# Kernel optimization log

Measured on AMD Instinct MI355X. Metric: run time of the kernel, lower is better.

## Reference

```python
import jax, jax.numpy as jnp
import numpy as np

PAD_IDX = 1
B, L, E, H = 2, 256, 512, 8
D = E // H
SCALE = D ** -0.5


def setup_inputs() -> dict:
    key = jax.random.key(0)
    ks = jax.random.split(key, 10)
    std = 0.02
    return {
        "queries": jax.random.normal(ks[0], (B, L, E), jnp.float32),
        "keys": jax.random.normal(ks[1], (B, L, E), jnp.float32),
        "values": jax.random.normal(ks[2], (B, L, E), jnp.float32),
        "relation": jax.random.normal(ks[3], (B, L, L, E), jnp.float32),
        "adj_mask": jax.random.randint(ks[4], (B, L, L), 0, 2, jnp.int32),
        "Wq": jax.random.normal(ks[5], (E, E), jnp.float32) * std,
        "bq": jnp.zeros((E,), jnp.float32),
        "Wk": jax.random.normal(ks[6], (E, E), jnp.float32) * std,
        "bk": jnp.zeros((E,), jnp.float32),
        "Wv": jax.random.normal(ks[7], (E, E), jnp.float32) * std,
        "bv": jnp.zeros((E,), jnp.float32),
        "Wr": jax.random.normal(ks[8], (2 * E, E), jnp.float32) * std,
        "Wo": jax.random.normal(ks[9], (E, E), jnp.float32) * std,
        "bo": jnp.zeros((E,), jnp.float32),
    }


def reference(queries, keys, values, relation, adj_mask,
              Wq, bq, Wk, bk, Wv, bv, Wr, Wo, bo):
    b, t, _ = queries.shape
    s = keys.shape[1]
    # input projections (torch Linear: y = x @ W.T + b)
    q = ((queries @ Wq.T + bq) * SCALE).reshape(b, t, H, D)
    k = (keys @ Wk.T + bk).reshape(b, s, H, D)
    v = (values @ Wv.T + bv).reshape(b, s, H, D)
    # relation projection -> relation queries/keys, [b, t, s, H, D] then transpose(1,2)
    rel = relation @ Wr.T                              # [b, t, s, 2E]
    rq, rk = jnp.split(rel, 2, axis=-1)
    rq = rq.reshape(b, t, s, H, D).transpose(0, 2, 1, 3, 4)  # [b, s, t, H, D]
    rk = rk.reshape(b, t, s, H, D).transpose(0, 2, 1, 3, 4)
    # broadcasted relation bias (requires t == s, as in the original)
    qe = q[:, :, None] + rq                            # [b, t, s, H, D]
    ke = k[:, None] + rk                               # [b, t, s, H, D]
    attn = jnp.einsum('bijhn,bijhn->bijh', qe, ke)     # [b, t, s, H]
    pad = (adj_mask == PAD_IDX)[..., None]             # [b, t, s, 1]
    attn = jnp.where(pad, -jnp.inf, attn)
    attn_weights = jax.nn.softmax(attn, axis=2)
    out = jnp.einsum('bijh,bjhn->bihn', attn_weights, v).reshape(b, t, E)
    out = out @ Wo.T + bo
    return out, attn_weights
```

## Files before the change

### kernel.cpp

```cpp
#include <hip/hip_runtime.h>

typedef unsigned int uint32;
typedef __attribute__((ext_vector_type(8))) short bf16x8;
typedef __attribute__((ext_vector_type(4))) float f32x4;


__device__ __forceinline__ uint32 bf_rne(uint32 u) {
  return (u + 0x7fffu + ((u >> 16) & 1u)) >> 16;
}

__global__ void cvt_wr_kernel(const float* __restrict__ Wr, unsigned short* __restrict__ WrBf) {
  int idx = blockIdx.x * 256 + threadIdx.x;
  const uint4* src = (const uint4*)Wr;
  uint4 x = src[idx];
  uint2 o;
  o.x = bf_rne(x.x) | (bf_rne(x.y) << 16);
  o.y = bf_rne(x.z) | (bf_rne(x.w) << 16);
  ((uint2*)WrBf)[idx] = o;
}

__global__ __launch_bounds__(256) void proj_kernel(
    const float* __restrict__ X0, const float* __restrict__ W0, const float* __restrict__ b0, float* __restrict__ Y0,
    const float* __restrict__ X1, const float* __restrict__ W1, const float* __restrict__ b1, float* __restrict__ Y1,
    const float* __restrict__ X2, const float* __restrict__ W2, const float* __restrict__ b2, float* __restrict__ Y2,
    float scale0) {
  int z = blockIdx.z;
  const float* X = (z == 0) ? X0 : (z == 1) ? X1 : X2;
  const float* W = (z == 0) ? W0 : (z == 1) ? W1 : W2;
  const float* bias = (z == 0) ? b0 : (z == 1) ? b1 : b2;
  float* Y = (z == 0) ? Y0 : (z == 1) ? Y1 : Y2;
  float scale = (z == 0) ? scale0 : 1.0f;

  __shared__ float Xs[16][68];
  __shared__ float Ws[16][68];

  int tid = threadIdx.x;
  int tx = tid & 15, ty = tid >> 4;
  int m0 = blockIdx.x * 64, n0 = blockIdx.y * 64;

  float acc[4][4] = {};

  for (int k0 = 0; k0 < 512; k0 += 16) {
#pragma unroll
    for (int u = 0; u < 4; ++u) {
      int idx = tid + u * 256;
      int ml = idx >> 4, kl = idx & 15;
      Xs[kl][ml] = X[(size_t)(m0 + ml) * 512 + k0 + kl];
      Ws[kl][ml] = W[(size_t)(n0 + ml) * 512 + k0 + kl];
    }
    __syncthreads();
#pragma unroll
    for (int kk = 0; kk < 16; ++kk) {
      float4 a = *(const float4*)&Xs[kk][ty * 4];
      float4 w = *(const float4*)&Ws[kk][tx * 4];
      float av[4] = {a.x, a.y, a.z, a.w};
      float wv[4] = {w.x, w.y, w.z, w.w};
#pragma unroll
      for (int i = 0; i < 4; ++i)
#pragma unroll
        for (int jj = 0; jj < 4; ++jj)
          acc[i][jj] += av[i] * wv[jj];
    }
    __syncthreads();
  }
#pragma unroll
  for (int i = 0; i < 4; ++i) {
    int m = m0 + ty * 4 + i;
#pragma unroll
    for (int jj = 0; jj < 4; ++jj) {
      int n = n0 + tx * 4 + jj;
      Y[(size_t)m * 512 + n] = (acc[i][jj] + bias[n]) * scale;
    }
  }
}

__global__ __launch_bounds__(256, 2) void rel_score_kernel(
    const float* __restrict__ rel,
    const unsigned short* __restrict__ wrbf,
    const float* __restrict__ qws,
    const float* __restrict__ kws,
    float* __restrict__ attn)
{
  __shared__ unsigned short As[64 * 520];
  __shared__ float scores[4][4][64];

  const int tid = threadIdx.x;
  const int lane = tid & 63;
  const int wv = tid >> 6;
  const int mt = blockIdx.x;
  const int b = mt >> 10;
  const int j = (mt >> 2) & 255;
  const int i0 = (mt & 3) << 6;

  const float* Abase = rel + (size_t)mt * (64 * 512);

  const int t15 = lane & 15;
  const int kq = (lane >> 4) * 8;

  const unsigned short* bptr[4];
#pragma unroll
  for (int fc = 0; fc < 4; ++fc) {
    int g = (wv & 1) * 4 + fc;
    int wr_row = (g & 1) * 512 + (wv >> 1) * 64 + (g >> 1) * 16 + t15;
    bptr[fc] = wrbf + (size_t)wr_row * 512 + kq;
  }

  const int arow0 = tid >> 3;
  const int ak8 = (tid & 7) * 8;
  const uint4* aptr0 = (const uint4*)(Abase + (size_t)arow0 * 512 + ak8);
  const uint4* aptr1 = (const uint4*)(Abase + (size_t)(arow0 + 32) * 512 + ak8);

  f32x4 acc[4][4];

  auto epilogue = [&](int hp) {
    const int hthis = hp * 2 + (wv >> 1);
    const int dbase = (wv & 1) * 32;
    const float* qbase = qws + ((size_t)(b * 256 + i0)) * 512 + hthis * 64;
    const float* krow = kws + ((size_t)(b * 256 + j)) * 512 + hthis * 64;
    const int rgrp = lane >> 4;
#pragma unroll
    for (int fr = 0; fr < 4; ++fr) {
#pragma unroll
      for (int r = 0; r < 4; ++r) {
        int m = fr * 16 + rgrp * 4 + r;
        float s = 0.f;
#pragma unroll
        for (int p = 0; p < 2; ++p) {
          int d = dbase + p * 16 + t15;
          float qv = qbase[(size_t)m * 512 + d];
          float kv = krow[d];
          s += (qv + acc[fr][p * 2][r]) * (kv + acc[fr][p * 2 + 1][r]);
        }
        s += __shfl_xor(s, 1);
        s += __shfl_xor(s, 2);
        s += __shfl_xor(s, 4);
        s += __shfl_xor(s, 8);
        if (t15 == 0) scores[hp][wv][m] = s;
      }
    }
    __syncthreads();
    if (tid < 128) {
      int hl = tid >> 6, m = tid & 63;
      float sc = scores[hp][hl * 2][m] + scores[hp][hl * 2 + 1][m];
      attn[(((size_t)(b * 256 + i0 + m)) * 256 + j) * 8 + hp * 2 + hl] = sc;
    }
  };

#pragma unroll
  for (int a = 0; a < 4; ++a)
#pragma unroll
    for (int c = 0; c < 4; ++c)
      acc[a][c] = (f32x4){0.f, 0.f, 0.f, 0.f};

  uint4 p0 = aptr0[0];
  uint4 p1 = aptr0[1];
  uint4 p2 = aptr1[0];
  uint4 p3 = aptr1[1];

  for (int k = 0; k < 8; ++k) {
    const int k0 = k * 64;
    bf16x8 bfr[2][4];
#pragma unroll
    for (int kh = 0; kh < 2; ++kh)
#pragma unroll
      for (int fc = 0; fc < 4; ++fc)
        bfr[kh][fc] = *(const bf16x8*)(bptr[fc] + k0 + kh * 32);
    {
      uint4 o;
      o.x = (p0.y & 0xffff0000u) | (p0.x >> 16);
      o.y = (p0.w & 0xffff0000u) | (p0.z >> 16);
      o.z = (p1.y & 0xffff0000u) | (p1.x >> 16);
      o.w = (p1.w & 0xffff0000u) | (p1.z >> 16);
      *(uint4*)&As[arow0 * 520 + k0 + ak8] = o;
      o.x = (p2.y & 0xffff0000u) | (p2.x >> 16);
      o.y = (p2.w & 0xffff0000u) | (p2.z >> 16);
      o.z = (p3.y & 0xffff0000u) | (p3.x >> 16);
      o.w = (p3.w & 0xffff0000u) | (p3.z >> 16);
      *(uint4*)&As[(arow0 + 32) * 520 + k0 + ak8] = o;
    }
    if (k < 7) {
      const uint4* n0p = (const uint4*)((const float*)aptr0 + (k + 1) * 64);
      const uint4* n1p = (const uint4*)((const float*)aptr1 + (k + 1) * 64);
      p0 = n0p[0];
      p1 = n0p[1];
      p2 = n1p[0];
      p3 = n1p[1];
    }
    __syncthreads();
#pragma unroll
    for (int kh = 0; kh < 2; ++kh) {
      int kk = k0 + kh * 32 + kq;
      bf16x8 af[4];
#pragma unroll
      for (int fr = 0; fr < 4; ++fr)
        af[fr] = *(const bf16x8*)&As[(fr * 16 + t15) * 520 + kk];
#pragma unroll
      for (int fr = 0; fr < 4; ++fr)
#pragma unroll
        for (int fc = 0; fc < 4; ++fc)
          acc[fr][fc] = __builtin_amdgcn_mfma_f32_16x16x32_bf16(
              af[fr], bfr[kh][fc], acc[fr][fc], 0, 0, 0);
    }
  }
  epilogue(0);

  for (int hp = 1; hp < 4; ++hp) {
#pragma unroll
    for (int a = 0; a < 4; ++a)
#pragma unroll
      for (int c = 0; c < 4; ++c)
        acc[a][c] = (f32x4){0.f, 0.f, 0.f, 0.f};

    const int hofs = hp * 65536;

    bf16x8 bfr[2][4];
#pragma unroll
    for (int kh = 0; kh < 2; ++kh)
#pragma unroll
      for (int fc = 0; fc < 4; ++fc)
        bfr[kh][fc] = *(const bf16x8*)(bptr[fc] + hofs + kh * 32);

#pragma unroll
    for (int k = 0; k < 8; ++k) {
      const int k0 = k * 64;
      bf16x8 bnx[2][4];
      if (k < 7) {
#pragma unroll
        for (int kh = 0; kh < 2; ++kh)
#pragma unroll
          for (int fc = 0; fc < 4; ++fc)
            bnx[kh][fc] = *(const bf16x8*)(bptr[fc] + hofs + k0 + 64 + kh * 32);
      }
#pragma unroll
      for (int kh = 0; kh < 2; ++kh) {
        int kk = k0 + kh * 32 + kq;
        bf16x8 af[4];
#pragma unroll
        for (int fr = 0; fr < 4; ++fr)
          af[fr] = *(const bf16x8*)&As[(fr * 16 + t15) * 520 + kk];
#pragma unroll
        for (int fr = 0; fr < 4; ++fr)
#pragma unroll
          for (int fc = 0; fc < 4; ++fc)
            acc[fr][fc] = __builtin_amdgcn_mfma_f32_16x16x32_bf16(
                af[fr], bfr[kh][fc], acc[fr][fc], 0, 0, 0);
      }
      if (k < 7) {
#pragma unroll
        for (int kh = 0; kh < 2; ++kh)
#pragma unroll
          for (int fc = 0; fc < 4; ++fc)
            bfr[kh][fc] = bnx[kh][fc];
      }
    }
    epilogue(hp);
  }
}

__global__ __launch_bounds__(256) void softmax_av_kernel(
    float* __restrict__ attn, const int* __restrict__ adj,
    const float* __restrict__ vws, float* __restrict__ o1) {
  __shared__ float sl[2048];
  __shared__ int msk[256];
  int bi = blockIdx.x;
  int b = bi >> 8;
  float* base = attn + (size_t)bi * 2048;
  const int* abase = adj + (size_t)bi * 256;
  int tid = threadIdx.x;
#pragma unroll
  for (int u = 0; u < 8; ++u) sl[tid + u * 256] = base[tid + u * 256];
  msk[tid] = abase[tid];
  __syncthreads();
  int h = tid >> 5, l5 = tid & 31;
  float mx = -INFINITY;
#pragma unroll
  for (int u = 0; u < 8; ++u) {
    int jj = l5 + u * 32;
    if (msk[jj] != 1) mx = fmaxf(mx, sl[jj * 8 + h]);
  }
#pragma unroll
  for (int off = 16; off >= 1; off >>= 1) mx = fmaxf(mx, __shfl_xor(mx, off));
  float ev[8];
  float sum = 0.f;
#pragma unroll
  for (int u = 0; u < 8; ++u) {
    int jj = l5 + u * 32;
    float e = (msk[jj] != 1) ? __expf(sl[jj * 8 + h] - mx) : 0.f;
    ev[u] = e;
    sum += e;
  }
#pragma unroll
  for (int off = 16; off >= 1; off >>= 1) sum += __shfl_xor(sum, off);
  float inv = (sum > 0.f) ? (1.f / sum) : 0.f;
#pragma unroll
  for (int u = 0; u < 8; ++u) {
    int jj = l5 + u * 32;
    sl[jj * 8 + h] = ev[u] * inv;
  }
  __syncthreads();
#pragma unroll
  for (int u = 0; u < 8; ++u) base[tid + u * 256] = sl[tid + u * 256];
  const float* vbase = vws + (size_t)b * (256 * 512);
  int e0 = tid, e1 = tid + 256;
  int h0 = e0 >> 6, h1 = e1 >> 6;
  float a0 = 0.f, a1 = 0.f;
  for (int jj = 0; jj < 256; ++jj) {
    float w0 = sl[jj * 8 + h0];
    float w1 = sl[jj * 8 + h1];
    const float* vr = vbase + (size_t)jj * 512;
    a0 += w0 * vr[e0];
    a1 += w1 * vr[e1];
  }
  float* orow = o1 + (size_t)bi * 512;
  orow[e0] = a0;
  orow[e1] = a1;
}

extern "C" void kernel_launch(void* const* d_in, const int* in_sizes, int n_in,
                              void* d_out, int out_size, void* d_ws, size_t ws_size,
                              hipStream_t stream) {
  const float* queries = (const float*)d_in[0];
  const float* keys    = (const float*)d_in[1];
  const float* values  = (const float*)d_in[2];
  const float* relation = (const float*)d_in[3];
  const int*   adj     = (const int*)d_in[4];
  const float* Wq = (const float*)d_in[5];
  const float* bq = (const float*)d_in[6];
  const float* Wk = (const float*)d_in[7];
  const float* bk = (const float*)d_in[8];
  const float* Wv = (const float*)d_in[9];
  const float* bv = (const float*)d_in[10];
  const float* Wr = (const float*)d_in[11];
  const float* Wo = (const float*)d_in[12];
  const float* bo = (const float*)d_in[13];

  float* out  = (float*)d_out;
  float* attn = out + 262144;

  float* ws  = (float*)d_ws;
  float* qws = ws;
  float* kws = ws + 262144;
  float* vws = ws + 524288;
  float* o1  = ws + 786432;
  unsigned short* wrbf = (unsigned short*)(ws + 1048576);

  cvt_wr_kernel<<<dim3(512), dim3(256), 0, stream>>>(Wr, wrbf);

  proj_kernel<<<dim3(8, 8, 3), dim3(256), 0, stream>>>(
      queries, Wq, bq, qws,
      keys,    Wk, bk, kws,
      values,  Wv, bv, vws,
      0.125f);

  rel_score_kernel<<<dim3(2048), dim3(256), 0, stream>>>(relation, wrbf, qws, kws, attn);

  softmax_av_kernel<<<dim3(512), dim3(256), 0, stream>>>(attn, adj, vws, o1);

  proj_kernel<<<dim3(8, 8, 1), dim3(256), 0, stream>>>(
      o1, Wo, bo, out,
      nullptr, nullptr, nullptr, nullptr,
      nullptr, nullptr, nullptr, nullptr,
      1.0f);
}
```

Measured before the change: 738.3 us.

## Double rel_score block to 512 threads with XOR-swizzled LDS and deeper prefetch

The relation-score kernel now runs 8 waves per block instead of 4, so each block covers 4 heads per pass and needs two head passes instead of four. The A-tile stage drops the row padding in favour of an XOR swizzle on the LDS address to avoid bank conflicts. Global loads of the relation row are prefetched two k-steps ahead. The aim is more parallel MFMA work per staged tile and less serial per-head work, at the cost of higher register pressure and a launch bound of 4 blocks per CU that may force spills.

```diff
diff --git a/kernel.cpp b/kernel.cpp
--- a/kernel.cpp
+++ b/kernel.cpp
@@ -74,19 +74,20 @@
   }
 }
 
-__global__ __launch_bounds__(256, 2) void rel_score_kernel(
+__global__ __launch_bounds__(512, 4) void rel_score_kernel(
     const float* __restrict__ rel,
     const unsigned short* __restrict__ wrbf,
     const float* __restrict__ qws,
     const float* __restrict__ kws,
     float* __restrict__ attn)
 {
-  __shared__ unsigned short As[64 * 520];
-  __shared__ float scores[4][4][64];
+  __shared__ unsigned short As[64 * 512];
+  __shared__ float scores[2][8][64];
 
   const int tid = threadIdx.x;
   const int lane = tid & 63;
-  const int wv = tid >> 6;
+  const int w = tid >> 6;
+  const int wvl = w & 3;
   const int mt = blockIdx.x;
   const int b = mt >> 10;
   const int j = (mt >> 2) & 255;
@@ -96,27 +97,30 @@
 
   const int t15 = lane & 15;
   const int kq = (lane >> 4) * 8;
+  const int rswz = (t15 & 7) << 3;
 
   const unsigned short* bptr[4];
 #pragma unroll
   for (int fc = 0; fc < 4; ++fc) {
-    int g = (wv & 1) * 4 + fc;
-    int wr_row = (g & 1) * 512 + (wv >> 1) * 64 + (g >> 1) * 16 + t15;
+    int g = (wvl & 1) * 4 + fc;
+    int head0 = (w >> 2) * 2 + (wvl >> 1);
+    int wr_row = (g & 1) * 512 + head0 * 64 + (g >> 1) * 16 + t15;
     bptr[fc] = wrbf + (size_t)wr_row * 512 + kq;
   }
 
-  const int arow0 = tid >> 3;
+  const int arow = tid >> 3;
   const int ak8 = (tid & 7) * 8;
-  const uint4* aptr0 = (const uint4*)(Abase + (size_t)arow0 * 512 + ak8);
-  const uint4* aptr1 = (const uint4*)(Abase + (size_t)(arow0 + 32) * 512 + ak8);
+  const uint4* aq = (const uint4*)(Abase + (size_t)arow * 512 + ak8);
+  const int wbase = arow * 512 + ak8;
+  const int wswz = (arow & 7) << 3;
 
   f32x4 acc[4][4];
 
-  auto epilogue = [&](int hp) {
-    const int hthis = hp * 2 + (wv >> 1);
-    const int dbase = (wv & 1) * 32;
-    const float* qbase = qws + ((size_t)(b * 256 + i0)) * 512 + hthis * 64;
-    const float* krow = kws + ((size_t)(b * 256 + j)) * 512 + hthis * 64;
+  auto epilogue = [&](int p) {
+    const int head = (2 * p + (w >> 2)) * 2 + (wvl >> 1);
+    const int dbase = (wvl & 1) * 32;
+    const float* qbase = qws + ((size_t)(b * 256 + i0)) * 512 + head * 64;
+    const float* krow = kws + ((size_t)(b * 256 + j)) * 512 + head * 64;
     const int rgrp = lane >> 4;
 #pragma unroll
     for (int fr = 0; fr < 4; ++fr) {
@@ -125,24 +129,24 @@
         int m = fr * 16 + rgrp * 4 + r;
         float s = 0.f;
 #pragma unroll
-        for (int p = 0; p < 2; ++p) {
-          int d = dbase + p * 16 + t15;
+        for (int p2 = 0; p2 < 2; ++p2) {
+          int d = dbase + p2 * 16 + t15;
           float qv = qbase[(size_t)m * 512 + d];
           float kv = krow[d];
-          s += (qv + acc[fr][p * 2][r]) * (kv + acc[fr][p * 2 + 1][r]);
+          s += (qv + acc[fr][p2 * 2][r]) * (kv + acc[fr][p2 * 2 + 1][r]);
         }
         s += __shfl_xor(s, 1);
         s += __shfl_xor(s, 2);
         s += __shfl_xor(s, 4);
         s += __shfl_xor(s, 8);
-        if (t15 == 0) scores[hp][wv][m] = s;
+        if (t15 == 0) scores[p][w][m] = s;
       }
     }
     __syncthreads();
-    if (tid < 128) {
+    if (tid < 256) {
       int hl = tid >> 6, m = tid & 63;
-      float sc = scores[hp][hl * 2][m] + scores[hp][hl * 2 + 1][m];
-      attn[(((size_t)(b * 256 + i0 + m)) * 256 + j) * 8 + hp * 2 + hl] = sc;
+      float sc = scores[p][hl * 2][m] + scores[p][hl * 2 + 1][m];
+      attn[(((size_t)(b * 256 + i0 + m)) * 256 + j) * 8 + 4 * p + hl] = sc;
     }
   };
 
@@ -152,11 +156,10 @@
     for (int c = 0; c < 4; ++c)
       acc[a][c] = (f32x4){0.f, 0.f, 0.f, 0.f};
 
-  uint4 p0 = aptr0[0];
-  uint4 p1 = aptr0[1];
-  uint4 p2 = aptr1[0];
-  uint4 p3 = aptr1[1];
-
+  uint4 c0a = aq[0], c0b = aq[1];
+  uint4 c1a = aq[16], c1b = aq[17];
+
+#pragma unroll
   for (int k = 0; k < 8; ++k) {
     const int k0 = k * 64;
     bf16x8 bfr[2][4];
@@ -167,24 +170,17 @@
         bfr[kh][fc] = *(const bf16x8*)(bptr[fc] + k0 + kh * 32);
     {
       uint4 o;
-      o.x = (p0.y & 0xffff0000u) | (p0.x >> 16);
-      o.y = (p0.w & 0xffff0000u) | (p0.z >> 16);
-      o.z = (p1.y & 0xffff0000u) | (p1.x >> 16);
-      o.w = (p1.w & 0xffff0000u) | (p1.z >> 16);
-      *(uint4*)&As[arow0 * 520 + k0 + ak8] = o;
-      o.x = (p2.y & 0xffff0000u) | (p2.x >> 16);
-      o.y = (p2.w & 0xffff0000u) | (p2.z >> 16);
-      o.z = (p3.y & 0xffff0000u) | (p3.x >> 16);
-      o.w = (p3.w & 0xffff0000u) | (p3.z >> 16);
-      *(uint4*)&As[(arow0 + 32) * 520 + k0 + ak8] = o;
-    }
-    if (k < 7) {
-      const uint4* n0p = (const uint4*)((const float*)aptr0 + (k + 1) * 64);
-      const uint4* n1p = (const uint4*)((const float*)aptr1 + (k + 1) * 64);
-      p0 = n0p[0];
-      p1 = n0p[1];
-      p2 = n1p[0];
-      p3 = n1p[1];
+      o.x = (c0a.y & 0xffff0000u) | (c0a.x >> 16);
+      o.y = (c0a.w & 0xffff0000u) | (c0a.z >> 16);
+      o.z = (c0b.y & 0xffff0000u) | (c0b.x >> 16);
+      o.w = (c0b.w & 0xffff0000u) | (c0b.z >> 16);
+      *(uint4*)&As[(wbase + k0) ^ wswz] = o;
+    }
+    c0a = c1a;
+    c0b = c1b;
+    if (k < 6) {
+      c1a = aq[(k + 2) * 16];
+      c1b = aq[(k + 2) * 16 + 1];
     }
     __syncthreads();
 #pragma unroll
@@ -193,7 +189,7 @@
       bf16x8 af[4];
 #pragma unroll
       for (int fr = 0; fr < 4; ++fr)
-        af[fr] = *(const bf16x8*)&As[(fr * 16 + t15) * 520 + kk];
+        af[fr] = *(const bf16x8*)&As[((fr * 16 + t15) * 512 + kk) ^ rswz];
 #pragma unroll
       for (int fr = 0; fr < 4; ++fr)
 #pragma unroll
@@ -204,14 +200,14 @@
   }
   epilogue(0);
 
-  for (int hp = 1; hp < 4; ++hp) {
-#pragma unroll
-    for (int a = 0; a < 4; ++a)
-#pragma unroll
-      for (int c = 0; c < 4; ++c)
-        acc[a][c] = (f32x4){0.f, 0.f, 0.f, 0.f};
-
-    const int hofs = hp * 65536;
+#pragma unroll
+  for (int a = 0; a < 4; ++a)
+#pragma unroll
+    for (int c = 0; c < 4; ++c)
+      acc[a][c] = (f32x4){0.f, 0.f, 0.f, 0.f};
+
+  {
+    const int hofs = 131072;
 
     bf16x8 bfr[2][4];
 #pragma unroll
@@ -237,7 +233,7 @@
         bf16x8 af[4];
 #pragma unroll
         for (int fr = 0; fr < 4; ++fr)
-          af[fr] = *(const bf16x8*)&As[(fr * 16 + t15) * 520 + kk];
+          af[fr] = *(const bf16x8*)&As[((fr * 16 + t15) * 512 + kk) ^ rswz];
 #pragma unroll
         for (int fr = 0; fr < 4; ++fr)
 #pragma unroll
@@ -253,8 +249,8 @@
             bfr[kh][fc] = bnx[kh][fc];
       }
     }
-    epilogue(hp);
-  }
+  }
+  epilogue(1);
 }
 
 __global__ __launch_bounds__(256) void softmax_av_kernel(
@@ -352,7 +348,7 @@
       values,  Wv, bv, vws,
       0.125f);
 
-  rel_score_kernel<<<dim3(2048), dim3(256), 0, stream>>>(relation, wrbf, qws, kws, attn);
+  rel_score_kernel<<<dim3(2048), dim3(512), 0, stream>>>(relation, wrbf, qws, kws, attn);
 
   softmax_av_kernel<<<dim3(512), dim3(256), 0, stream>>>(attn, adj, vws, o1);
 
```

Result: slower. 818.0 us (+10.8%).
